# Kernel optimization log

Hardware: AMD Instinct MI355X
Metric: run time of the kernel (lower is better)

## Reference

```python
import jax, jax.numpy as jnp
import numpy as np

B, T, D, H = 4, 2048, 1024, 16
HD = D // H  # 64


def setup_inputs() -> dict:
    key = jax.random.key(0)
    ks = jax.random.split(key, 6)
    s = 0.02
    return {
        "embed": jax.random.normal(ks[0], (B, T, D), dtype=jnp.float32),
        "mask": jnp.ones((1, 1, 1, T), dtype=jnp.int32),
        "Wq": jax.random.normal(ks[1], (D, D), dtype=jnp.float32) * s,
        "bq": jnp.zeros((D,), dtype=jnp.float32),
        "Wk": jax.random.normal(ks[2], (D, D), dtype=jnp.float32) * s,
        "bk": jnp.zeros((D,), dtype=jnp.float32),
        "Wv": jax.random.normal(ks[3], (D, D), dtype=jnp.float32) * s,
        "bv": jnp.zeros((D,), dtype=jnp.float32),
        "Wo": jax.random.normal(ks[4], (D, D), dtype=jnp.float32) * s,
        "bo": jnp.zeros((D,), dtype=jnp.float32),
    }


def _attn(embed, Wq, bq, Wk, bk, Wv, bv, Wo, bo, mask):
    b, t, _ = embed.shape
    q = (embed @ Wq + bq).reshape(b, t, H, HD).transpose(0, 2, 1, 3)  # [B,H,T,hd]
    k = (embed @ Wk + bk).reshape(b, t, H, HD).transpose(0, 2, 1, 3)
    v = (embed @ Wv + bv).reshape(b, t, H, HD).transpose(0, 2, 1, 3)
    scores = jnp.einsum("bhqd,bhkd->bhqk", q, k) * (1.0 / np.sqrt(HD))
    scores = jnp.where(mask == 0, jnp.float32(-jnp.inf), scores)
    weights = jax.nn.softmax(scores, axis=-1)  # dropout p=0 in eval
    ctx = jnp.einsum("bhqk,bhkd->bhqd", weights, v)
    merged = ctx.transpose(0, 2, 1, 3).reshape(b, t, D)
    return merged @ Wo + bo


def reference(embed, mask, Wq, bq, Wk, bk, Wv, bv, Wo, bo):
    return _attn(embed, Wq, bq, Wk, bk, Wv, bv, Wo, bo, mask)
```

## Files before the change

### kernel.cpp

```cpp
#include <hip/hip_runtime.h>


typedef __bf16 bf16_t;
typedef bf16_t bf16x8 __attribute__((ext_vector_type(8)));
typedef float  f32x4  __attribute__((ext_vector_type(4)));
typedef unsigned u32x4 __attribute__((ext_vector_type(4)));
typedef unsigned short u16x8 __attribute__((ext_vector_type(8)));
typedef unsigned short u16x4 __attribute__((ext_vector_type(4)));

#define DEV static __device__ __forceinline__

constexpr int Bc = 4, Tc = 2048, Dc = 1024, Hc = 16, HDc = 64;
constexpr int Mc = Bc * Tc;
constexpr int NQKV = 3 * Dc;

DEV unsigned short f2bf(float f) {
  union { float f; unsigned u; } v; v.f = f;
  return (unsigned short)((v.u + 0x7fffu + ((v.u >> 16) & 1u)) >> 16);
}

DEV void gload_lds16(const void* g, const void* ldsbase) {
  unsigned m0v = __builtin_amdgcn_readfirstlane((unsigned)(unsigned long long)ldsbase);
  asm volatile("s_mov_b32 m0, %0\n\t"
               "global_load_lds_dwordx4 %1, off"
               :: "s"(m0v), "v"(g) : "memory");
}

DEV f32x4 mfma16(bf16x8 a, bf16x8 b, f32x4 c) {
  return __builtin_amdgcn_mfma_f32_16x16x32_bf16(a, b, c, 0, 0, 0);
}

DEV void pl32swap(unsigned& a, unsigned& b) {
  asm("v_permlane32_swap_b32 %0, %1" : "+v"(a), "+v"(b));
}
DEV void pl16swap(unsigned& a, unsigned& b) {
  asm("v_permlane16_swap_b32 %0, %1" : "+v"(a), "+v"(b));
}

DEV int fragaddr(int row, int col) {
  return (row >> 4) * 1024 + ((col >> 5) << 9) + (((col >> 3) & 3) << 7)
       + ((row & 15) << 3) + (col & 7);
}

__global__ __launch_bounds__(256) void prep(const float* __restrict__ embed,
                                            const float* __restrict__ Wq,
                                            const float* __restrict__ Wk,
                                            const float* __restrict__ Wv,
                                            const float* __restrict__ Wo,
                                            const float* __restrict__ bq,
                                            const float* __restrict__ bk,
                                            const float* __restrict__ bv,
                                            unsigned short* __restrict__ embed_bf,
                                            unsigned short* __restrict__ WtAll,
                                            float* __restrict__ ball) {
  __shared__ unsigned short tile[64 * 80];
  const int bb = blockIdx.x;
  const int tid = threadIdx.x;

  if (bb < 8192) {
    int i = bb * 256 + tid;
    float4 v = ((const float4*)embed)[i];
    u16x4 o = { f2bf(v.x), f2bf(v.y), f2bf(v.z), f2bf(v.w) };
    *(u16x4*)(embed_bf + (size_t)i * 4) = o;
    return;
  }
  if (bb < 8192 + 1024) {
    int wb = bb - 8192;
    int bx = wb & 15, by = (wb >> 4) & 15, bz = wb >> 8;
    const float* W = bz == 0 ? Wq : bz == 1 ? Wk : bz == 2 ? Wv : Wo;
    unsigned short* dst = WtAll + (size_t)bz * 1024 * 1024;
    const int kb = by * 64, nb = bx * 64;
#pragma unroll
    for (int i = 0; i < 4; i++) {
      int ci = i * 256 + tid;
      int r = ci >> 4, c4 = ci & 15;
      float4 v = *(const float4*)(W + (size_t)(kb + r) * 1024 + nb + c4 * 4);
      u16x4 o = { f2bf(v.x), f2bf(v.y), f2bf(v.z), f2bf(v.w) };
      *(u16x4*)(tile + r * 80 + c4 * 4) = o;
    }
    __syncthreads();
#pragma unroll
    for (int i = 0; i < 2; i++) {
      int ci = i * 256 + tid;
      int n = ci >> 3, c8 = ci & 7;
      u16x8 o;
#pragma unroll
      for (int j = 0; j < 8; j++) o[j] = tile[(c8 * 8 + j) * 80 + n];
      *(u16x8*)(dst + (size_t)(nb + n) * 1024 + kb + c8 * 8) = o;
    }
    return;
  }
#pragma unroll
  for (int it = 0; it < 12; it++) {
    int i = it * 256 + tid;
    ball[i] = (i < 1024) ? bq[i] : (i < 2048) ? bk[i - 1024] : bv[i - 2048];
  }
}

template <int OUTMODE>
__global__ __launch_bounds__(256) void gemm_bt(const unsigned short* __restrict__ A,
                                               const unsigned short* __restrict__ Bt,
                                               const float* __restrict__ bias,
                                               void* __restrict__ Cout,
                                               unsigned short* __restrict__ Kf,
                                               unsigned short* __restrict__ Vf,
                                               int N, int K) {
  __shared__ unsigned short As[128 * 64];
  __shared__ unsigned short Bs[128 * 64];
  const int tid = threadIdx.x;
  const int lane = tid & 63, wid = tid >> 6;
  const int lr = lane & 15, lg = lane >> 4;
  const int wrow = wid >> 1, wcol = wid & 1;
  const int m0 = blockIdx.y * 128, n0 = blockIdx.x * 128;

  f32x4 acc[4][4] = {};

  for (int k0 = 0; k0 < K; k0 += 64) {
#pragma unroll
    for (int i = 0; i < 4; i++) {
      int ci = i * 256 + tid;
      int row = ci >> 3, ph = ci & 7;
      int cl = ph ^ (row & 7);
      gload_lds16(A + (size_t)(m0 + row) * K + k0 + cl * 8, As + (size_t)(i * 256 + wid * 64) * 8);
      gload_lds16(Bt + (size_t)(n0 + row) * K + k0 + cl * 8, Bs + (size_t)(i * 256 + wid * 64) * 8);
    }
    asm volatile("s_waitcnt vmcnt(0)" ::: "memory");
    __syncthreads();
#pragma unroll
    for (int kk = 0; kk < 2; kk++) {
      bf16x8 av[4], bv[4];
#pragma unroll
      for (int m = 0; m < 4; m++) {
        int row = wrow * 64 + m * 16 + lr;
        int ph = (kk * 4 + lg) ^ (row & 7);
        av[m] = *(const bf16x8*)(As + row * 64 + ph * 8);
      }
#pragma unroll
      for (int n = 0; n < 4; n++) {
        int row = wcol * 64 + n * 16 + lr;
        int ph = (kk * 4 + lg) ^ (row & 7);
        bv[n] = *(const bf16x8*)(Bs + row * 64 + ph * 8);
      }
#pragma unroll
      for (int m = 0; m < 4; m++)
#pragma unroll
        for (int n = 0; n < 4; n++)
          acc[m][n] = mfma16(av[m], bv[n], acc[m][n]);
    }
    __syncthreads();
  }

#pragma unroll
  for (int m = 0; m < 4; m++)
#pragma unroll
    for (int n = 0; n < 4; n++)
#pragma unroll
      for (int r = 0; r < 4; r++) {
        int row = m0 + wrow * 64 + m * 16 + lg * 4 + r;
        int col = n0 + wcol * 64 + n * 16 + lr;
        float v = acc[m][n][r] + bias[col];
        if (OUTMODE == 1) {
          int b = row >> 11, tl = row & 2047;
          if (col < Dc) {
            v *= 0.18033688f;
            int h = col >> 6, d = col & 63;
            ((unsigned short*)Cout)[(size_t)(b * 16 + h) * 131072 + fragaddr(tl, d)] = f2bf(v);
          } else if (col < 2 * Dc) {
            int c = col - Dc, h = c >> 6, d = c & 63;
            Kf[(size_t)(b * 16 + h) * 131072 + fragaddr(tl, d)] = f2bf(v);
          } else {
            int c = col - 2 * Dc, h = c >> 6, d = c & 63;
            Vf[(size_t)(b * 16 + h) * 131072 + (tl >> 6) * 4096 + fragaddr(d, tl & 63)] = f2bf(v);
          }
        } else {
          ((float*)Cout)[(size_t)row * N + col] = v;
        }
      }
}

__global__ __launch_bounds__(256, 3) void flash6(const unsigned short* __restrict__ Qf,
                                                 const unsigned short* __restrict__ Kf,
                                                 const unsigned short* __restrict__ Vf,
                                                 const int* __restrict__ mask,
                                                 unsigned short* __restrict__ merged) {
  const int tid = threadIdx.x;
  const int lane = tid & 63, wid = tid >> 6;
  const int lr = lane & 15, lg = lane >> 4;

  const int lin = blockIdx.y * 16 + blockIdx.x;
  const int swz = (lin & 7) * 128 + (lin >> 3);
  const int qb = swz & 15, bh = swz >> 4;
  const int b = bh >> 4, h = bh & 15;
  const int wq = qb * 128 + wid * 32;

  const unsigned short* Qb = Qf + (size_t)bh * 131072;
  const unsigned short* Kb = Kf + (size_t)bh * 131072;
  const unsigned short* Vb = Vf + (size_t)bh * 131072;

  bf16x8 qf[2][2];
#pragma unroll
  for (int qn = 0; qn < 2; qn++)
#pragma unroll
    for (int kk = 0; kk < 2; kk++)
      qf[qn][kk] = *(const bf16x8*)(Qb + ((wq >> 4) + qn) * 1024 + kk * 512 + lane * 8);

  f32x4 o[2][4] = {};
  f32x4 lacc[2] = {};

  bf16x8 ones;
#pragma unroll
  for (int j = 0; j < 8; j++) ones[j] = (bf16_t)1.0f;

  bool allone = true;
#pragma unroll
  for (int j = 0; j < 8; j++) {
    int4 mv = ((const int4*)mask)[j * 64 + lane];
    allone = allone && (mv.x != 0) && (mv.y != 0) && (mv.z != 0) && (mv.w != 0);
  }
  const bool nomask = (__ballot(allone) == ~0ull);

#pragma unroll 2
  for (int tile = 0; tile < 32; tile++) {
    bf16x8 kf[4][2];
#pragma unroll
    for (int n = 0; n < 4; n++)
#pragma unroll
      for (int kk = 0; kk < 2; kk++)
        kf[n][kk] = *(const bf16x8*)(Kb + (tile * 4 + n) * 1024 + kk * 512 + lane * 8);
    bf16x8 vf[4][2];
#pragma unroll
    for (int dn = 0; dn < 4; dn++)
#pragma unroll
      for (int kk = 0; kk < 2; kk++)
        vf[dn][kk] = *(const bf16x8*)(Vb + tile * 4096 + dn * 1024 + kk * 512 + lane * 8);

    unsigned long long mb = ~0ull;
    if (!nomask) mb = __ballot(mask[tile * 64 + lane] != 0);

    unsigned pk[2][4][2];
#pragma unroll
    for (int kvn = 0; kvn < 4; kvn++) {
      f32x4 st[2] = {};
#pragma unroll
      for (int qn = 0; qn < 2; qn++) {
        st[qn] = mfma16(kf[kvn][0], qf[qn][0], st[qn]);
        st[qn] = mfma16(kf[kvn][1], qf[qn][1], st[qn]);
      }
      if (mb != ~0ull) {
#pragma unroll
        for (int r = 0; r < 4; r++)
          if (!((mb >> (kvn * 16 + lg * 4 + r)) & 1ull)) {
#pragma unroll
            for (int qn = 0; qn < 2; qn++) st[qn][r] = -1e30f;
          }
      }
#pragma unroll
      for (int qn = 0; qn < 2; qn++) {
        float e[4];
#pragma unroll
        for (int r = 0; r < 4; r++)
          asm("v_exp_f32 %0, %1" : "=v"(e[r]) : "v"(st[qn][r]));
        asm("v_cvt_pk_bf16_f32 %0, %1, %2" : "=v"(pk[qn][kvn][0]) : "v"(e[0]), "v"(e[1]));
        asm("v_cvt_pk_bf16_f32 %0, %1, %2" : "=v"(pk[qn][kvn][1]) : "v"(e[2]), "v"(e[3]));
      }
    }

    bf16x8 pa[2][2];
#pragma unroll
    for (int qn = 0; qn < 2; qn++)
#pragma unroll
      for (int m = 0; m < 2; m++) {
        unsigned a0 = pk[qn][2 * m][0], b0 = pk[qn][2 * m + 1][0];
        unsigned a1 = pk[qn][2 * m][1], b1 = pk[qn][2 * m + 1][1];
        pl32swap(a0, b0);
        pl32swap(a1, b1);
        pl16swap(a0, b0);
        pl16swap(a1, b1);
        u32x4 w = { a0, a1, b0, b1 };
        pa[qn][m] = __builtin_bit_cast(bf16x8, w);
      }

    __builtin_amdgcn_s_setprio(1);
#pragma unroll
    for (int qn = 0; qn < 2; qn++) {
#pragma unroll
      for (int dn = 0; dn < 4; dn++) {
        o[qn][dn] = mfma16(pa[qn][0], vf[dn][0], o[qn][dn]);
        o[qn][dn] = mfma16(pa[qn][1], vf[dn][1], o[qn][dn]);
      }
      lacc[qn] = mfma16(pa[qn][0], ones, lacc[qn]);
      lacc[qn] = mfma16(pa[qn][1], ones, lacc[qn]);
    }
    __builtin_amdgcn_s_setprio(0);
  }

#pragma unroll
  for (int qn = 0; qn < 2; qn++)
#pragma unroll
    for (int r = 0; r < 4; r++) {
      float inv = 1.0f / lacc[qn][r];
      int grow = b * Tc + wq + qn * 16 + lg * 4 + r;
#pragma unroll
      for (int dn = 0; dn < 4; dn++) {
        int gcol = h * HDc + dn * 16 + lr;
        merged[(size_t)grow * Dc + gcol] = f2bf(o[qn][dn][r] * inv);
      }
    }
}

extern "C" void kernel_launch(void* const* d_in, const int* in_sizes, int n_in,
                              void* d_out, int out_size, void* d_ws, size_t ws_size,
                              hipStream_t stream) {
  const float* embed = (const float*)d_in[0];
  const int*   mask  = (const int*)d_in[1];
  const float* Wq = (const float*)d_in[2];
  const float* bq = (const float*)d_in[3];
  const float* Wk = (const float*)d_in[4];
  const float* bk = (const float*)d_in[5];
  const float* Wv = (const float*)d_in[6];
  const float* bv = (const float*)d_in[7];
  const float* Wo = (const float*)d_in[8];
  const float* bo = (const float*)d_in[9];
  float* out = (float*)d_out;

  char* ws = (char*)d_ws;
  unsigned short* embed_bf = (unsigned short*)ws; ws += (size_t)Mc * Dc * 2;
  unsigned short* WtAll    = (unsigned short*)ws; ws += (size_t)4 * Dc * Dc * 2;
  float*          ball     = (float*)ws;          ws += 16384;
  unsigned short* Qf       = (unsigned short*)ws; ws += (size_t)Mc * Dc * 2;
  unsigned short* Kf       = (unsigned short*)ws; ws += (size_t)Mc * Dc * 2;
  unsigned short* Vf       = (unsigned short*)ws; ws += (size_t)Mc * Dc * 2;
  unsigned short* merged   = (unsigned short*)ws; ws += (size_t)Mc * Dc * 2;

  prep<<<8192 + 1024 + 1, 256, 0, stream>>>(embed, Wq, Wk, Wv, Wo, bq, bk, bv,
                                            embed_bf, WtAll, ball);
  gemm_bt<1><<<dim3(24, 64), 256, 0, stream>>>(embed_bf, WtAll, ball, Qf, Kf, Vf, NQKV, Dc);
  flash6<<<dim3(16, 64), 256, 0, stream>>>(Qf, Kf, Vf, mask, merged);
  gemm_bt<0><<<dim3(8, 64), 256, 0, stream>>>(merged, WtAll + (size_t)3 * Dc * Dc, bo, out, nullptr, nullptr, Dc, Dc);
}
```

Measured before the change: 205.5 us.

## Add 256x256-tile QKV GEMM with 4-stage async LDS pipeline

Replaces the templated 128x128 QKV projection GEMM with a dedicated 512-thread kernel computing 256x256 tiles. It uses a 4-buffer, 3-deep prefetch pipeline with direct global-to-LDS loads, explicit vmcnt waits, raw barriers, s_setprio around MFMA bursts, and a block swizzle for L2 locality. The aim is to hide load latency and raise data reuse per tile, at the cost of 128KB of LDS and high register pressure. The output GEMM is simplified to a plain fp32 store path.

```diff
diff --git a/kernel.cpp b/kernel.cpp
--- a/kernel.cpp
+++ b/kernel.cpp
@@ -97,13 +97,143 @@
   }
 }
 
-template <int OUTMODE>
+__global__ __launch_bounds__(512, 2) void gemm_qkv8(
+    const unsigned short* __restrict__ A,
+    const unsigned short* __restrict__ Bt,
+    const float* __restrict__ bias,
+    unsigned short* __restrict__ Qf,
+    unsigned short* __restrict__ Kf,
+    unsigned short* __restrict__ Vf) {
+  __shared__ unsigned short As_[4 * 8192];
+  __shared__ unsigned short Bs_[4 * 8192];
+
+  const int tid = threadIdx.x;
+  const int lane = tid & 63, wid = tid >> 6;
+  const int lr = lane & 15, lg = lane >> 4;
+  const int wr = wid >> 2, wc = wid & 3;
+
+  const int lin = blockIdx.y * 12 + blockIdx.x;
+  const int swz = (lin & 7) * 48 + (lin >> 3);
+  const int m0 = (swz / 12) * 256, n0 = (swz % 12) * 256;
+
+  size_t gA[2], gB[2];
+  int ldsoff[2];
+#pragma unroll
+  for (int i = 0; i < 2; i++) {
+    int ci = i * 512 + tid;
+    int row = ci >> 2;
+    int cl = (ci & 3) ^ (row & 3);
+    gA[i] = (size_t)(m0 + row) * 1024 + cl * 8;
+    gB[i] = (size_t)(n0 + row) * 1024 + cl * 8;
+    ldsoff[i] = ci * 8;
+  }
+
+  int offA[2][4], offB[4];
+#pragma unroll
+  for (int mq = 0; mq < 2; mq++)
+#pragma unroll
+    for (int m = 0; m < 4; m++) {
+      int row = wr * 128 + mq * 64 + m * 16 + lr;
+      offA[mq][m] = row * 32 + ((lg ^ (row & 3)) << 3);
+    }
+#pragma unroll
+  for (int n = 0; n < 4; n++) {
+    int row = wc * 64 + n * 16 + lr;
+    offB[n] = row * 32 + ((lg ^ (row & 3)) << 3);
+  }
+
+  f32x4 acc[8][4] = {};
+
+#define QSTAGE(kt) {                                                         \
+    const int sbi_ = (kt) & 3;                                               \
+    _Pragma("unroll")                                                        \
+    for (int i_ = 0; i_ < 2; i_++) {                                         \
+      gload_lds16(A  + gA[i_] + (size_t)(kt) * 32,                           \
+                  As_ + sbi_ * 8192 + ldsoff[i_]);                           \
+      gload_lds16(Bt + gB[i_] + (size_t)(kt) * 32,                           \
+                  Bs_ + sbi_ * 8192 + ldsoff[i_]);                           \
+    } }
+
+#define QKTILE(kt, VM, DOST) {                                               \
+    const int bi_ = (kt) & 3;                                                \
+    const unsigned short* Ab = As_ + bi_ * 8192;                             \
+    const unsigned short* Bb = Bs_ + bi_ * 8192;                             \
+    asm volatile("s_waitcnt vmcnt(" VM ")" ::: "memory");                    \
+    asm volatile("s_barrier" ::: "memory");                                  \
+    bf16x8 a0 = *(const bf16x8*)(Ab + offA[0][0]);                           \
+    bf16x8 a1 = *(const bf16x8*)(Ab + offA[0][1]);                           \
+    bf16x8 a2 = *(const bf16x8*)(Ab + offA[0][2]);                           \
+    bf16x8 a3 = *(const bf16x8*)(Ab + offA[0][3]);                           \
+    bf16x8 b0 = *(const bf16x8*)(Bb + offB[0]);                              \
+    bf16x8 b1 = *(const bf16x8*)(Bb + offB[1]);                              \
+    bf16x8 b2 = *(const bf16x8*)(Bb + offB[2]);                              \
+    bf16x8 b3 = *(const bf16x8*)(Bb + offB[3]);                              \
+    if (DOST) QSTAGE((kt) + 3);                                              \
+    __builtin_amdgcn_s_setprio(1);                                           \
+    acc[0][0]=mfma16(a0,b0,acc[0][0]); acc[0][1]=mfma16(a0,b1,acc[0][1]);    \
+    acc[0][2]=mfma16(a0,b2,acc[0][2]); acc[0][3]=mfma16(a0,b3,acc[0][3]);    \
+    acc[1][0]=mfma16(a1,b0,acc[1][0]); acc[1][1]=mfma16(a1,b1,acc[1][1]);    \
+    acc[1][2]=mfma16(a1,b2,acc[1][2]); acc[1][3]=mfma16(a1,b3,acc[1][3]);    \
+    acc[2][0]=mfma16(a2,b0,acc[2][0]); acc[2][1]=mfma16(a2,b1,acc[2][1]);    \
+    acc[2][2]=mfma16(a2,b2,acc[2][2]); acc[2][3]=mfma16(a2,b3,acc[2][3]);    \
+    acc[3][0]=mfma16(a3,b0,acc[3][0]); acc[3][1]=mfma16(a3,b1,acc[3][1]);    \
+    acc[3][2]=mfma16(a3,b2,acc[3][2]); acc[3][3]=mfma16(a3,b3,acc[3][3]);    \
+    __builtin_amdgcn_s_setprio(0);                                           \
+    a0 = *(const bf16x8*)(Ab + offA[1][0]);                                  \
+    a1 = *(const bf16x8*)(Ab + offA[1][1]);                                  \
+    a2 = *(const bf16x8*)(Ab + offA[1][2]);                                  \
+    a3 = *(const bf16x8*)(Ab + offA[1][3]);                                  \
+    __builtin_amdgcn_s_setprio(1);                                           \
+    acc[4][0]=mfma16(a0,b0,acc[4][0]); acc[4][1]=mfma16(a0,b1,acc[4][1]);    \
+    acc[4][2]=mfma16(a0,b2,acc[4][2]); acc[4][3]=mfma16(a0,b3,acc[4][3]);    \
+    acc[5][0]=mfma16(a1,b0,acc[5][0]); acc[5][1]=mfma16(a1,b1,acc[5][1]);    \
+    acc[5][2]=mfma16(a1,b2,acc[5][2]); acc[5][3]=mfma16(a1,b3,acc[5][3]);    \
+    acc[6][0]=mfma16(a2,b0,acc[6][0]); acc[6][1]=mfma16(a2,b1,acc[6][1]);    \
+    acc[6][2]=mfma16(a2,b2,acc[6][2]); acc[6][3]=mfma16(a2,b3,acc[6][3]);    \
+    acc[7][0]=mfma16(a3,b0,acc[7][0]); acc[7][1]=mfma16(a3,b1,acc[7][1]);    \
+    acc[7][2]=mfma16(a3,b2,acc[7][2]); acc[7][3]=mfma16(a3,b3,acc[7][3]);    \
+    __builtin_amdgcn_s_setprio(0); }
+
+  QSTAGE(0); QSTAGE(1); QSTAGE(2);
+
+#pragma unroll 1
+  for (int kt = 0; kt < 29; ++kt) {
+    QKTILE(kt, "8", 1);
+  }
+  QKTILE(29, "8", 0);
+  QKTILE(30, "4", 0);
+  QKTILE(31, "0", 0);
+#undef QSTAGE
+#undef QKTILE
+
+#pragma unroll
+  for (int mq = 0; mq < 8; mq++)
+#pragma unroll
+    for (int n = 0; n < 4; n++)
+#pragma unroll
+      for (int r = 0; r < 4; r++) {
+        int row = m0 + wr * 128 + (mq >> 2) * 64 + (mq & 3) * 16 + lg * 4 + r;
+        int col = n0 + wc * 64 + n * 16 + lr;
+        float v = acc[mq][n][r] + bias[col];
+        int bb = row >> 11, tl = row & 2047;
+        if (col < Dc) {
+          v *= 0.18033688f;
+          int h = col >> 6, d = col & 63;
+          Qf[(size_t)(bb * 16 + h) * 131072 + fragaddr(tl, d)] = f2bf(v);
+        } else if (col < 2 * Dc) {
+          int c = col - Dc, h = c >> 6, d = c & 63;
+          Kf[(size_t)(bb * 16 + h) * 131072 + fragaddr(tl, d)] = f2bf(v);
+        } else {
+          int c = col - 2 * Dc, h = c >> 6, d = c & 63;
+          Vf[(size_t)(bb * 16 + h) * 131072 + (tl >> 6) * 4096 + fragaddr(d, tl & 63)] = f2bf(v);
+        }
+      }
+}
+
 __global__ __launch_bounds__(256) void gemm_bt(const unsigned short* __restrict__ A,
                                                const unsigned short* __restrict__ Bt,
                                                const float* __restrict__ bias,
-                                               void* __restrict__ Cout,
-                                               unsigned short* __restrict__ Kf,
-                                               unsigned short* __restrict__ Vf,
+                                               float* __restrict__ Cout,
                                                int N, int K) {
   __shared__ unsigned short As[128 * 64];
   __shared__ unsigned short Bs[128 * 64];
@@ -158,23 +288,7 @@
       for (int r = 0; r < 4; r++) {
         int row = m0 + wrow * 64 + m * 16 + lg * 4 + r;
         int col = n0 + wcol * 64 + n * 16 + lr;
-        float v = acc[m][n][r] + bias[col];
-        if (OUTMODE == 1) {
-          int b = row >> 11, tl = row & 2047;
-          if (col < Dc) {
-            v *= 0.18033688f;
-            int h = col >> 6, d = col & 63;
-            ((unsigned short*)Cout)[(size_t)(b * 16 + h) * 131072 + fragaddr(tl, d)] = f2bf(v);
-          } else if (col < 2 * Dc) {
-            int c = col - Dc, h = c >> 6, d = c & 63;
-            Kf[(size_t)(b * 16 + h) * 131072 + fragaddr(tl, d)] = f2bf(v);
-          } else {
-            int c = col - 2 * Dc, h = c >> 6, d = c & 63;
-            Vf[(size_t)(b * 16 + h) * 131072 + (tl >> 6) * 4096 + fragaddr(d, tl & 63)] = f2bf(v);
-          }
-        } else {
-          ((float*)Cout)[(size_t)row * N + col] = v;
-        }
+        Cout[(size_t)row * N + col] = acc[m][n][r] + bias[col];
       }
 }
 
@@ -334,7 +448,7 @@
 
   prep<<<8192 + 1024 + 1, 256, 0, stream>>>(embed, Wq, Wk, Wv, Wo, bq, bk, bv,
                                             embed_bf, WtAll, ball);
-  gemm_bt<1><<<dim3(24, 64), 256, 0, stream>>>(embed_bf, WtAll, ball, Qf, Kf, Vf, NQKV, Dc);
+  gemm_qkv8<<<dim3(12, 32), 512, 0, stream>>>(embed_bf, WtAll, ball, Qf, Kf, Vf);
   flash6<<<dim3(16, 64), 256, 0, stream>>>(Qf, Kf, Vf, mask, merged);
-  gemm_bt<0><<<dim3(8, 64), 256, 0, stream>>>(merged, WtAll + (size_t)3 * Dc * Dc, bo, out, nullptr, nullptr, Dc, Dc);
-}
+  gemm_bt<<<dim3(8, 64), 256, 0, stream>>>(merged, WtAll + (size_t)3 * Dc * Dc, bo, out, Dc, Dc);
+}
```

Measured after the change: 204.2 us. About the same (-0.6%).
